# Performance work log

Measured on AMD Instinct MI355X. Metric: run time of the kernel, lower is better.

The kernel has to match this reference:

```python
import jax, jax.numpy as jnp
import numpy as np

ATTWSIZE = 64  # sliding window length (matches init_kwargs attwsize)


def setup_inputs() -> dict:
    key = jax.random.key(0)
    k1, k2, k3 = jax.random.split(key, 3)
    B, T, D, A = 32, 4096, 256, 128
    x = jax.random.normal(k1, (B, T, D), dtype=jnp.float32)
    Wp = jax.random.normal(k2, (A, D), dtype=jnp.float32) / np.sqrt(D).astype(np.float32)
    bp = jnp.zeros((A,), dtype=jnp.float32)
    Wg = jax.random.normal(k3, (1, A), dtype=jnp.float32) / np.sqrt(A).astype(np.float32)
    return {"x": x, "Wp": Wp, "bp": bp, "Wg": Wg}


def _windowed_sum(v, w):
    # causal sliding-window sum over axis=1: sum(v[:, max(t-w+1,0):t+1, :])
    # single-pass cumsum formulation: cs[t] - cs[t-w]
    cs = jnp.cumsum(v, axis=1)
    T = v.shape[1]
    shifted = jnp.pad(cs, ((0, 0), (w, 0), (0, 0)))[:, :T, :]
    return cs - shifted


def reference(x, Wp, bp, Wg):
    # proj = tanh(Linear(dimio->dimatt)(x))
    proj = jnp.tanh(jnp.einsum('btd,ad->bta', x, Wp) + bp)
    # gvec = sigmoid(Linear(dimatt->1, no bias)(proj))  -> [B, T, 1]
    g = jax.nn.sigmoid(jnp.einsum('bta,oa->bto', proj, Wg))
    wx = g * x  # gated input [B, T, D]
    num = _windowed_sum(wx, ATTWSIZE)         # [B, T, D]
    den = _windowed_sum(g, ATTWSIZE)          # [B, T, 1] broadcasts over D
    return num / den
```

## Files before the change

### kernel.cpp

```cpp
#include <hip/hip_runtime.h>

#define TT 4096
#define DD 256
#define AA 128
#define WIN 64

typedef short bf16x8 __attribute__((ext_vector_type(8)));
typedef float f32x4 __attribute__((ext_vector_type(4)));

__device__ __forceinline__ unsigned short f2bf(float f) {
    unsigned int u = __builtin_bit_cast(unsigned int, f);
    u += 0x7FFFu + ((u >> 16) & 1u);
    return (unsigned short)(u >> 16);
}

__global__ __launch_bounds__(256) void prep_wp(const float* __restrict__ Wp,
                                               unsigned short* __restrict__ wpb) {
    int i = blockIdx.x * 256 + threadIdx.x;
    wpb[i] = f2bf(Wp[i]);
}

#define LDK 264
#define RTILE 128
#define NSUB 2

__global__ __launch_bounds__(256, 3) void gate_kernel(
        const float* __restrict__ x, const unsigned short* __restrict__ wpb,
        const float* __restrict__ bp, const float* __restrict__ Wg,
        float* __restrict__ g) {
    __shared__ unsigned short xs[64 * LDK];
    __shared__ float psum[4][64];
    const int tid  = threadIdx.x;
    const int lane = tid & 63;
    const int wave = tid >> 6;
    const int quad = lane >> 4;
    const int nrow = lane & 15;
    const long row0 = (long)blockIdx.x * RTILE;

    bf16x8 bfrag[2][8];
    float bpv[2], wgv[2];
#pragma unroll
    for (int nt = 0; nt < 2; ++nt) {
        int n = wave * 32 + nt * 16 + nrow;
        bpv[nt] = bp[n];
        wgv[nt] = Wg[n];
#pragma unroll
        for (int k0 = 0; k0 < 8; ++k0)
            bfrag[nt][k0] = *reinterpret_cast<const bf16x8*>(
                wpb + n * DD + k0 * 32 + quad * 8);
    }

    for (int s = 0; s < NSUB; ++s) {
        const float* xsrc = x + (row0 + s * 64) * DD;
#pragma unroll
        for (int it = 0; it < 16; ++it) {
            int idx = it * 256 + tid;
            int r   = idx >> 6;
            int c4  = idx & 63;
            float4 v = reinterpret_cast<const float4*>(xsrc + r * DD)[c4];
            ushort4 h;
            h.x = f2bf(v.x); h.y = f2bf(v.y); h.z = f2bf(v.z); h.w = f2bf(v.w);
            *reinterpret_cast<ushort4*>(&xs[r * LDK + c4 * 4]) = h;
        }
        __syncthreads();

        f32x4 acc[4][2];
#pragma unroll
        for (int mt = 0; mt < 4; ++mt)
#pragma unroll
            for (int nt = 0; nt < 2; ++nt)
                acc[mt][nt] = (f32x4){0.f, 0.f, 0.f, 0.f};

#pragma unroll
        for (int k0 = 0; k0 < 8; ++k0) {
#pragma unroll
            for (int mt = 0; mt < 4; ++mt) {
                bf16x8 af = *reinterpret_cast<const bf16x8*>(
                    &xs[(mt * 16 + nrow) * LDK + quad * 8 + k0 * 32]);
                acc[mt][0] = __builtin_amdgcn_mfma_f32_16x16x32_bf16(af, bfrag[0][k0], acc[mt][0], 0, 0, 0);
                acc[mt][1] = __builtin_amdgcn_mfma_f32_16x16x32_bf16(af, bfrag[1][k0], acc[mt][1], 0, 0, 0);
            }
        }

        float p[4][4];
#pragma unroll
        for (int mt = 0; mt < 4; ++mt)
#pragma unroll
            for (int r = 0; r < 4; ++r) p[mt][r] = 0.f;
#pragma unroll
        for (int nt = 0; nt < 2; ++nt) {
#pragma unroll
            for (int mt = 0; mt < 4; ++mt) {
#pragma unroll
                for (int r = 0; r < 4; ++r) {
                    float pre = acc[mt][nt][r] + bpv[nt];
                    float e  = __expf(2.0f * pre);
                    float th = 1.0f - 2.0f * __builtin_amdgcn_rcpf(e + 1.0f);
                    p[mt][r] += th * wgv[nt];
                }
            }
        }
#pragma unroll
        for (int off = 1; off <= 8; off <<= 1)
#pragma unroll
            for (int mt = 0; mt < 4; ++mt)
#pragma unroll
                for (int r = 0; r < 4; ++r)
                    p[mt][r] += __shfl_xor(p[mt][r], off, 64);
        if (nrow == 0) {
#pragma unroll
            for (int mt = 0; mt < 4; ++mt)
#pragma unroll
                for (int r = 0; r < 4; ++r)
                    psum[wave][mt * 16 + quad * 4 + r] = p[mt][r];
        }
        __syncthreads();
        if (tid < 64) {
            float ssum = psum[0][tid] + psum[1][tid] + psum[2][tid] + psum[3][tid];
            g[row0 + s * 64 + tid] = __builtin_amdgcn_rcpf(1.0f + __expf(-ssum));
        }
        __syncthreads();
    }
}

#define TC 128
#define NCHUNK (TT / TC)

__global__ __launch_bounds__(256) void stream_kernel(
        const float* __restrict__ x, const float* __restrict__ g,
        float* __restrict__ out) {
    __shared__ float gbuf[TC + WIN];
    const int b     = blockIdx.x >> 5;
    const int chunk = blockIdx.x & (NCHUNK - 1);
    const int t0    = chunk * TC;
    const int d     = threadIdx.x;
    const float* xb = x + (size_t)b * TT * DD;
    const float* gb = g + (size_t)b * TT;
    float* ob = out + (size_t)b * TT * DD;

    if (d < TC + WIN) {
        int s = t0 - WIN + d;
        gbuf[d] = (s >= 0) ? gb[s] : 0.f;
    }
    __syncthreads();

    float S = 0.f, Sg = 0.f;
#pragma unroll 16
    for (int i = 0; i < WIN; ++i) {
        int s  = t0 - WIN + i;
        int sc = s < 0 ? 0 : s;
        float gv = gbuf[i];
        S  += gv * xb[(size_t)sc * DD + d];
        Sg += gv;
    }

#pragma unroll 8
    for (int tt = 0; tt < TC; ++tt) {
        int t  = t0 + tt;
        int ts = t - WIN;
        int tsc = ts < 0 ? 0 : ts;
        float gnew = gbuf[WIN + tt];
        float gold = gbuf[tt];
        float vnew = gnew * xb[(size_t)t * DD + d];
        float vold = gold * xb[(size_t)tsc * DD + d];
        S  += vnew - vold;
        Sg += gnew - gold;
        ob[(size_t)t * DD + d] = S * __builtin_amdgcn_rcpf(Sg);
    }
}

extern "C" void kernel_launch(void* const* d_in, const int* in_sizes, int n_in,
                              void* d_out, int out_size, void* d_ws, size_t ws_size,
                              hipStream_t stream) {
    const float* x  = (const float*)d_in[0];
    const float* Wp = (const float*)d_in[1];
    const float* bp = (const float*)d_in[2];
    const float* Wg = (const float*)d_in[3];
    float* out = (float*)d_out;

    unsigned short* wpb = (unsigned short*)d_ws;
    float* g = (float*)((char*)d_ws + 65536);

    prep_wp<<<AA * DD / 256, 256, 0, stream>>>(Wp, wpb);
    gate_kernel<<<32 * TT / RTILE, 256, 0, stream>>>(x, wpb, bp, Wg, g);
    stream_kernel<<<32 * NCHUNK, 256, 0, stream>>>(x, g, out);
}
```

Baseline: 309.9 us.

## Double-buffer gate kernel x tiles via async LDS loads and vectorize stream kernel

The gate kernel now stages fp32 x rows straight into swizzled shared memory with asynchronous global-to-LDS loads, double-buffered across smaller 32-row subtiles. The bf16 conversion moves to the point where fragments are read, using packed convert instructions. The aim is to overlap global loads with MFMA work and drop the register round-trip, at the cost of twice the LDS footprint and lower occupancy. Separately, the stream kernel processes two adjacent channels per thread with float2 accesses and two time chunks per block, to cut instruction overhead.

```diff
diff --git a/kernel.cpp b/kernel.cpp
--- a/kernel.cpp
+++ b/kernel.cpp
@@ -7,6 +7,7 @@
 
 typedef short bf16x8 __attribute__((ext_vector_type(8)));
 typedef float f32x4 __attribute__((ext_vector_type(4)));
+typedef unsigned int u32x4 __attribute__((ext_vector_type(4)));
 
 __device__ __forceinline__ unsigned short f2bf(float f) {
     unsigned int u = __builtin_bit_cast(unsigned int, f);
@@ -14,28 +15,36 @@
     return (unsigned short)(u >> 16);
 }
 
+__device__ __forceinline__ unsigned int cvt_pk_bf16(float lo, float hi) {
+    unsigned int r;
+    asm("v_cvt_pk_bf16_f32 %0, %1, %2" : "=v"(r) : "v"(lo), "v"(hi));
+    return r;
+}
+
 __global__ __launch_bounds__(256) void prep_wp(const float* __restrict__ Wp,
                                                unsigned short* __restrict__ wpb) {
     int i = blockIdx.x * 256 + threadIdx.x;
     wpb[i] = f2bf(Wp[i]);
 }
 
-#define LDK 264
 #define RTILE 128
-#define NSUB 2
-
-__global__ __launch_bounds__(256, 3) void gate_kernel(
+#define SROWS 32
+#define NSUB  (RTILE / SROWS)
+
+__global__ __launch_bounds__(256, 2) void gate_kernel(
         const float* __restrict__ x, const unsigned short* __restrict__ wpb,
         const float* __restrict__ bp, const float* __restrict__ Wg,
         float* __restrict__ g) {
-    __shared__ unsigned short xs[64 * LDK];
-    __shared__ float psum[4][64];
+    __shared__ __align__(16) float xs[2][SROWS * DD];
+    __shared__ float psum[4][SROWS];
     const int tid  = threadIdx.x;
     const int lane = tid & 63;
     const int wave = tid >> 6;
     const int quad = lane >> 4;
     const int nrow = lane & 15;
+    const int sw   = nrow & 7;
     const long row0 = (long)blockIdx.x * RTILE;
+    const float* xbase = x + row0 * DD;
 
     bf16x8 bfrag[2][8];
     float bpv[2], wgv[2];
@@ -50,23 +59,29 @@
                 wpb + n * DD + k0 * 32 + quad * 8);
     }
 
+    auto stage = [&](int nb, int s) {
+        const float* src = xbase + (long)s * SROWS * DD;
+#pragma unroll
+        for (int j = 0; j < 8; ++j) {
+            int r = wave * 8 + j;
+            const float* gp = src + r * DD + ((lane ^ (r & 7)) << 2);
+            __builtin_amdgcn_global_load_lds(
+                (const __attribute__((address_space(1))) void*)gp,
+                (__attribute__((address_space(3))) void*)&xs[nb][r * DD],
+                16, 0, 0);
+        }
+    };
+
+    stage(0, 0);
+    __syncthreads();
+
     for (int s = 0; s < NSUB; ++s) {
-        const float* xsrc = x + (row0 + s * 64) * DD;
-#pragma unroll
-        for (int it = 0; it < 16; ++it) {
-            int idx = it * 256 + tid;
-            int r   = idx >> 6;
-            int c4  = idx & 63;
-            float4 v = reinterpret_cast<const float4*>(xsrc + r * DD)[c4];
-            ushort4 h;
-            h.x = f2bf(v.x); h.y = f2bf(v.y); h.z = f2bf(v.z); h.w = f2bf(v.w);
-            *reinterpret_cast<ushort4*>(&xs[r * LDK + c4 * 4]) = h;
-        }
-        __syncthreads();
-
-        f32x4 acc[4][2];
-#pragma unroll
-        for (int mt = 0; mt < 4; ++mt)
+        if (s + 1 < NSUB) stage((s + 1) & 1, s + 1);
+        const int cur = s & 1;
+
+        f32x4 acc[2][2];
+#pragma unroll
+        for (int mt = 0; mt < 2; ++mt)
 #pragma unroll
             for (int nt = 0; nt < 2; ++nt)
                 acc[mt][nt] = (f32x4){0.f, 0.f, 0.f, 0.f};
@@ -74,23 +89,31 @@
 #pragma unroll
         for (int k0 = 0; k0 < 8; ++k0) {
 #pragma unroll
-            for (int mt = 0; mt < 4; ++mt) {
-                bf16x8 af = *reinterpret_cast<const bf16x8*>(
-                    &xs[(mt * 16 + nrow) * LDK + quad * 8 + k0 * 32]);
+            for (int mt = 0; mt < 2; ++mt) {
+                const float* rowp = &xs[cur][(mt * 16 + nrow) * DD];
+                const int gidx = quad * 2 + k0 * 8;
+                float4 f0 = *reinterpret_cast<const float4*>(rowp + (((gidx)     ^ sw) << 2));
+                float4 f1 = *reinterpret_cast<const float4*>(rowp + (((gidx + 1) ^ sw) << 2));
+                u32x4 w;
+                w.x = cvt_pk_bf16(f0.x, f0.y);
+                w.y = cvt_pk_bf16(f0.z, f0.w);
+                w.z = cvt_pk_bf16(f1.x, f1.y);
+                w.w = cvt_pk_bf16(f1.z, f1.w);
+                bf16x8 af = __builtin_bit_cast(bf16x8, w);
                 acc[mt][0] = __builtin_amdgcn_mfma_f32_16x16x32_bf16(af, bfrag[0][k0], acc[mt][0], 0, 0, 0);
                 acc[mt][1] = __builtin_amdgcn_mfma_f32_16x16x32_bf16(af, bfrag[1][k0], acc[mt][1], 0, 0, 0);
             }
         }
 
-        float p[4][4];
-#pragma unroll
-        for (int mt = 0; mt < 4; ++mt)
+        float p[2][4];
+#pragma unroll
+        for (int mt = 0; mt < 2; ++mt)
 #pragma unroll
             for (int r = 0; r < 4; ++r) p[mt][r] = 0.f;
 #pragma unroll
         for (int nt = 0; nt < 2; ++nt) {
 #pragma unroll
-            for (int mt = 0; mt < 4; ++mt) {
+            for (int mt = 0; mt < 2; ++mt) {
 #pragma unroll
                 for (int r = 0; r < 4; ++r) {
                     float pre = acc[mt][nt][r] + bpv[nt];
@@ -103,21 +126,21 @@
 #pragma unroll
         for (int off = 1; off <= 8; off <<= 1)
 #pragma unroll
-            for (int mt = 0; mt < 4; ++mt)
+            for (int mt = 0; mt < 2; ++mt)
 #pragma unroll
                 for (int r = 0; r < 4; ++r)
                     p[mt][r] += __shfl_xor(p[mt][r], off, 64);
         if (nrow == 0) {
 #pragma unroll
-            for (int mt = 0; mt < 4; ++mt)
+            for (int mt = 0; mt < 2; ++mt)
 #pragma unroll
                 for (int r = 0; r < 4; ++r)
                     psum[wave][mt * 16 + quad * 4 + r] = p[mt][r];
         }
         __syncthreads();
-        if (tid < 64) {
+        if (tid < SROWS) {
             float ssum = psum[0][tid] + psum[1][tid] + psum[2][tid] + psum[3][tid];
-            g[row0 + s * 64 + tid] = __builtin_amdgcn_rcpf(1.0f + __expf(-ssum));
+            g[row0 + s * SROWS + tid] = __builtin_amdgcn_rcpf(1.0f + __expf(-ssum));
         }
         __syncthreads();
     }
@@ -129,43 +152,51 @@
 __global__ __launch_bounds__(256) void stream_kernel(
         const float* __restrict__ x, const float* __restrict__ g,
         float* __restrict__ out) {
-    __shared__ float gbuf[TC + WIN];
-    const int b     = blockIdx.x >> 5;
-    const int chunk = blockIdx.x & (NCHUNK - 1);
+    __shared__ float gbuf[2][TC + WIN];
+    const int grp  = threadIdx.x >> 7;
+    const int d2   = threadIdx.x & 127;
+    const int pair = blockIdx.x * 2 + grp;
+    const int b     = pair >> 5;
+    const int chunk = pair & (NCHUNK - 1);
     const int t0    = chunk * TC;
-    const int d     = threadIdx.x;
-    const float* xb = x + (size_t)b * TT * DD;
-    const float* gb = g + (size_t)b * TT;
-    float* ob = out + (size_t)b * TT * DD;
-
-    if (d < TC + WIN) {
-        int s = t0 - WIN + d;
-        gbuf[d] = (s >= 0) ? gb[s] : 0.f;
+    const float2* xb2 = reinterpret_cast<const float2*>(x + (size_t)b * TT * DD);
+    const float*  gb  = g + (size_t)b * TT;
+    float2* ob2 = reinterpret_cast<float2*>(out + (size_t)b * TT * DD);
+
+    for (int i = d2; i < TC + WIN; i += 128) {
+        int s = t0 - WIN + i;
+        gbuf[grp][i] = (s >= 0) ? gb[s] : 0.f;
     }
     __syncthreads();
 
-    float S = 0.f, Sg = 0.f;
+    float2 S = {0.f, 0.f};
+    float Sg = 0.f;
 #pragma unroll 16
     for (int i = 0; i < WIN; ++i) {
         int s  = t0 - WIN + i;
         int sc = s < 0 ? 0 : s;
-        float gv = gbuf[i];
-        S  += gv * xb[(size_t)sc * DD + d];
-        Sg += gv;
+        float gv = gbuf[grp][i];
+        float2 xv = xb2[(size_t)sc * (DD / 2) + d2];
+        S.x += gv * xv.x;
+        S.y += gv * xv.y;
+        Sg  += gv;
     }
 
 #pragma unroll 8
     for (int tt = 0; tt < TC; ++tt) {
-        int t  = t0 + tt;
-        int ts = t - WIN;
+        int t   = t0 + tt;
+        int ts  = t - WIN;
         int tsc = ts < 0 ? 0 : ts;
-        float gnew = gbuf[WIN + tt];
-        float gold = gbuf[tt];
-        float vnew = gnew * xb[(size_t)t * DD + d];
-        float vold = gold * xb[(size_t)tsc * DD + d];
-        S  += vnew - vold;
-        Sg += gnew - gold;
-        ob[(size_t)t * DD + d] = S * __builtin_amdgcn_rcpf(Sg);
+        float gnew = gbuf[grp][WIN + tt];
+        float gold = gbuf[grp][tt];
+        float2 xn = xb2[(size_t)t   * (DD / 2) + d2];
+        float2 xo = xb2[(size_t)tsc * (DD / 2) + d2];
+        S.x += gnew * xn.x - gold * xo.x;
+        S.y += gnew * xn.y - gold * xo.y;
+        Sg  += gnew - gold;
+        float r = __builtin_amdgcn_rcpf(Sg);
+        float2 o; o.x = S.x * r; o.y = S.y * r;
+        ob2[(size_t)t * (DD / 2) + d2] = o;
     }
 }
 
@@ -183,5 +214,5 @@
 
     prep_wp<<<AA * DD / 256, 256, 0, stream>>>(Wp, wpb);
     gate_kernel<<<32 * TT / RTILE, 256, 0, stream>>>(x, wpb, bp, Wg, g);
-    stream_kernel<<<32 * NCHUNK, 256, 0, stream>>>(x, g, out);
-}
+    stream_kernel<<<32 * NCHUNK / 2, 256, 0, stream>>>(x, g, out);
+}
```

Measured after the change: 299.5 us. -3.4%, faster.
